# Kernel tuning notes

Hardware: AMD Instinct MI355X
Metric: run time of the kernel (lower is better)

## Reference

```python
import jax, jax.numpy as jnp
import numpy as np

G = 56          # voxel grid resolution per axis
N = 65536
K = 27          # 3x3x3 kernel offsets
C_IN = 128
C_OUT = 128


def _build_rulebook():
    """Submanifold conv rulebook: for each kernel offset, (input_row, output_row) pairs.

    Padded to P=N pairs per offset; invalid pairs use in_idx=0 and out_idx=N
    (a dummy output slot that is dropped), so shapes are static.
    """
    rng = np.random.default_rng(0)
    keys = np.sort(rng.choice(G ** 3, size=N, replace=False)).astype(np.int64)
    x = keys // (G * G)
    y = (keys // G) % G
    z = keys % G
    in_idx = np.zeros((K, N), dtype=np.int32)
    out_idx = np.full((K, N), N, dtype=np.int32)
    k = 0
    for dx in (-1, 0, 1):
        for dy in (-1, 0, 1):
            for dz in (-1, 0, 1):
                nx, ny, nz = x + dx, y + dy, z + dz
                valid = (nx >= 0) & (nx < G) & (ny >= 0) & (ny < G) & (nz >= 0) & (nz < G)
                nkey = (nx * G + ny) * G + nz
                pos = np.searchsorted(keys, np.clip(nkey, 0, G ** 3 - 1))
                pos = np.clip(pos, 0, N - 1)
                found = valid & (keys[pos] == nkey)
                cnt = int(found.sum())
                in_idx[k, :cnt] = pos[found]
                out_idx[k, :cnt] = np.nonzero(found)[0]
                k += 1
    return jnp.asarray(in_idx), jnp.asarray(out_idx)


def setup_inputs() -> dict:
    key = jax.random.key(0)
    k1, k2, k3 = jax.random.split(key, 3)
    fan_in = K * C_IN
    features = jax.random.normal(k1, (N, C_IN), dtype=jnp.float32)
    weight = jax.random.normal(k2, (K, C_IN, C_OUT), dtype=jnp.float32) * (1.0 / np.sqrt(fan_in))
    bias = jax.random.normal(k3, (C_OUT,), dtype=jnp.float32) * 0.01
    in_idx, out_idx = _build_rulebook()
    return {"features": features, "weight": weight, "bias": bias,
            "in_idx": in_idx, "out_idx": out_idx}


def reference(features, weight, bias, in_idx, out_idx):
    # gather: [K, P, C_in]
    gathered = features[in_idx]
    # per-offset GEMM: [K, P, C_out]
    contrib = jnp.einsum('kpc,kcd->kpd', gathered, weight)
    n = features.shape[0]
    c_out = weight.shape[-1]
    # scatter-accumulate into N real rows + 1 dummy row for padded pairs
    out = jnp.zeros((n + 1, c_out), dtype=features.dtype)
    out = out.at[out_idx.reshape(-1)].add(contrib.reshape(-1, c_out))
    return out[:n] + bias
```

## Files before the change

### kernel.cpp

```cpp
#include <hip/hip_runtime.h>
#include <hip/hip_bf16.h>
#include <stdint.h>

#define NV   65536
#define KOFF 27
#define CIN  128
#define COUT 128

typedef __bf16 bf16x8 __attribute__((ext_vector_type(8)));
typedef float  f32x4  __attribute__((ext_vector_type(4)));

__device__ __forceinline__ void async_copy16(void* lds, const void* g) {
    __builtin_amdgcn_global_load_lds(
        (const __attribute__((address_space(1))) void*)g,
        (__attribute__((address_space(3))) void*)lds,
        16, 0, 0);
}

#define JOB_A_BLOCKS 4097
#define JOB_B_BLOCKS 432
#define JOB_S_BLOCKS 1728

__global__ void k_prep_all(const float* __restrict__ f,
                           uint4* __restrict__ fb4,
                           const float* __restrict__ w,
                           uint4* __restrict__ wfrag4,
                           const int4* __restrict__ in4,
                           const int4* __restrict__ out4,
                           int* __restrict__ nbr) {
    const int b = blockIdx.x;
    const int t = threadIdx.x;
    if (b < JOB_A_BLOCKS) {
        int i = b * 256 + t;
        int total8  = (NV + 1) * CIN / 8;
        int nvalid8 = NV * CIN / 8;
        if (i >= total8) return;
        union { uint4 u; __hip_bfloat16 h[8]; } p;
        if (i < nvalid8) {
            const float4* f4 = (const float4*)f;
            float4 a = f4[i * 2];
            float4 c = f4[i * 2 + 1];
            p.h[0] = __float2bfloat16(a.x);
            p.h[1] = __float2bfloat16(a.y);
            p.h[2] = __float2bfloat16(a.z);
            p.h[3] = __float2bfloat16(a.w);
            p.h[4] = __float2bfloat16(c.x);
            p.h[5] = __float2bfloat16(c.y);
            p.h[6] = __float2bfloat16(c.z);
            p.h[7] = __float2bfloat16(c.w);
        } else {
            p.u = make_uint4(0, 0, 0, 0);
        }
        fb4[i] = p.u;
    } else if (b < JOB_A_BLOCKS + JOB_B_BLOCKS) {
        int c    = (b - JOB_A_BLOCKS) * 256 + t;
        int lane = c & 63;
        int nt   = (c >> 6) & 3;
        int wv   = (c >> 8) & 3;
        int s    = c >> 10;
        int ks   = s & 3;
        int k    = s >> 2;
        int cout = (wv & 1) * 64 + nt * 16 + (lane & 15);
        int cin0 = ks * 32 + (lane >> 4) * 8;
        const float* wk = w + k * 16384;
        union { uint4 u; __hip_bfloat16 h[8]; } p;
        #pragma unroll
        for (int j = 0; j < 8; ++j)
            p.h[j] = __float2bfloat16(wk[(cin0 + j) * 128 + cout]);
        wfrag4[c] = p.u;
    } else {
        int i = (b - JOB_A_BLOCKS - JOB_B_BLOCKS) * 256 + t;
        int k = i >> 14;
        int4 ii = in4[i];
        int4 oo = out4[i];
        int* nb = nbr + k * (NV + 1);
        nb[oo.x] = ii.x;
        nb[oo.y] = ii.y;
        nb[oo.z] = ii.z;
        nb[oo.w] = ii.w;
    }
}

__global__ __launch_bounds__(256, 2)
void sp_conv_main(const __hip_bfloat16* __restrict__ feats,
                  const uint4* __restrict__ wfrag,
                  const int* __restrict__ nbr,
                  const float* __restrict__ bias,
                  float* __restrict__ out) {
    __shared__ unsigned char smem[65536];

    const int t   = threadIdx.x;
    const int bid = blockIdx.x;
    const int tile0 = ((bid & 7) * 64 + (bid >> 3)) * 128;

    const int w    = t >> 6;
    const int lane = t & 63;
    const int lr   = lane & 15;
    const int quad = lane >> 4;
    const int m0   = (w >> 1) * 64;
    const int n0   = (w & 1) * 64;

    const int srow   = t >> 4;
    const int sbyte  = ((t & 15) ^ srow) * 16;

    f32x4 acc[4][4] = {};

    const unsigned char* featsB = (const unsigned char*)feats;

    int arows[8];
    {
        const int* nbr0 = nbr + tile0;
        #pragma unroll
        for (int i = 0; i < 8; ++i) arows[i] = nbr0[i * 16 + srow];
    }
    #pragma unroll
    for (int i = 0; i < 8; ++i) {
        unsigned ar = min((unsigned)arows[i], (unsigned)NV);
        async_copy16(smem + i * 4096 + t * 16,
                     featsB + (size_t)ar * 256 + sbyte);
    }
    {
        const int* nbr1 = nbr + (NV + 1) + tile0;
        #pragma unroll
        for (int i = 0; i < 8; ++i) arows[i] = nbr1[i * 16 + srow];
    }
    const uint4* wfp = wfrag + w * 256 + lane;
    uint4 bb[2][4];
    #pragma unroll
    for (int nt = 0; nt < 4; ++nt) bb[0][nt] = wfp[nt * 64];
    __syncthreads();

    int cbuf = 0;
    for (int k = 0; k < KOFF; ++k) {
        if (k + 1 < KOFF) {
            unsigned char* dst = smem + (cbuf ^ 1) * 32768;
            #pragma unroll
            for (int i = 0; i < 8; ++i) {
                unsigned ar = min((unsigned)arows[i], (unsigned)NV);
                async_copy16(dst + i * 4096 + t * 16,
                             featsB + (size_t)ar * 256 + sbyte);
            }
            if (k + 2 < KOFF) {
                const int* nbrn = nbr + (k + 2) * (NV + 1) + tile0;
                #pragma unroll
                for (int i = 0; i < 8; ++i) arows[i] = nbrn[i * 16 + srow];
            }
        }

        const unsigned char* base = smem + cbuf * 32768;
        #pragma unroll
        for (int ks = 0; ks < 4; ++ks) {
            const int s = k * 4 + ks;
            if (s + 1 < 4 * KOFF) {
                const uint4* wfn = wfp + (size_t)(s + 1) * 1024;
                #pragma unroll
                for (int nt = 0; nt < 4; ++nt)
                    bb[(ks + 1) & 1][nt] = wfn[nt * 64];
            }
            bf16x8 af[4];
            #pragma unroll
            for (int mt = 0; mt < 4; ++mt) {
                int row = m0 + mt * 16 + lr;
                af[mt] = *(const bf16x8*)(base + row * 256 +
                                          (((ks * 4 + quad) ^ lr) * 16));
            }
            #pragma unroll
            for (int mt = 0; mt < 4; ++mt)
                #pragma unroll
                for (int nt = 0; nt < 4; ++nt)
                    acc[mt][nt] = __builtin_amdgcn_mfma_f32_16x16x32_bf16(
                        af[mt], *(const bf16x8*)&bb[ks & 1][nt],
                        acc[mt][nt], 0, 0, 0);
        }
        __syncthreads();
        cbuf ^= 1;
    }

    float bv[4];
    #pragma unroll
    for (int nt = 0; nt < 4; ++nt) bv[nt] = bias[n0 + nt * 16 + lr];

    #pragma unroll
    for (int mt = 0; mt < 4; ++mt) {
        #pragma unroll
        for (int nt = 0; nt < 4; ++nt) {
            #pragma unroll
            for (int r = 0; r < 4; ++r) {
                int grow = tile0 + m0 + mt * 16 + quad * 4 + r;
                out[(size_t)grow * COUT + n0 + nt * 16 + lr] =
                    acc[mt][nt][r] + bv[nt];
            }
        }
    }
}


extern "C" void kernel_launch(void* const* d_in, const int* in_sizes, int n_in,
                              void* d_out, int out_size, void* d_ws, size_t ws_size,
                              hipStream_t stream) {
    const float* features = (const float*)d_in[0];
    const float* weight   = (const float*)d_in[1];
    const float* bias     = (const float*)d_in[2];
    const int*   in_idx   = (const int*)d_in[3];
    const int*   out_idx  = (const int*)d_in[4];
    float* out = (float*)d_out;

    uint8_t* ws = (uint8_t*)d_ws;
    size_t off = 0;
    __hip_bfloat16* feats_bf = (__hip_bfloat16*)(ws + off);
    off += (size_t)(NV + 1) * CIN * 2;
    off = (off + 255) & ~(size_t)255;
    uint4* wfrag = (uint4*)(ws + off);
    off += (size_t)(4 * KOFF) * 1024 * 16;
    off = (off + 255) & ~(size_t)255;
    int* nbr = (int*)(ws + off);

    hipMemsetAsync(nbr, 0xFF, (size_t)KOFF * (NV + 1) * 4, stream);

    k_prep_all<<<JOB_A_BLOCKS + JOB_B_BLOCKS + JOB_S_BLOCKS, 256, 0, stream>>>(
        features, (uint4*)feats_bf, weight, wfrag,
        (const int4*)in_idx, (const int4*)out_idx, nbr);

    sp_conv_main<<<NV / 128, 256, 0, stream>>>(feats_bf, wfrag, nbr, bias, out);
}
```

Measured before the change: 165.7 us.

## Prefetch whole-offset weight fragments a stage ahead and dedupe weight layout

The weight fragment buffer drops its duplicated copies for the two waves sharing an N-half, which halves the prep work and workspace. The main loop is unrolled by two with ping-pong register buffers. All four k-slices of the next offset's weight fragments are loaded one offset ahead instead of one k-slice ahead, hiding more global-load latency behind the MFMAs. In exchange, register use roughly quadruples for B fragments (32 uint4 per thread), which risks spills or lower occupancy under launch_bounds(256,2).

```diff
diff --git a/kernel.cpp b/kernel.cpp
--- a/kernel.cpp
+++ b/kernel.cpp
@@ -18,7 +18,7 @@
 }
 
 #define JOB_A_BLOCKS 4097
-#define JOB_B_BLOCKS 432
+#define JOB_B_BLOCKS 216
 #define JOB_S_BLOCKS 1728
 
 __global__ void k_prep_all(const float* __restrict__ f,
@@ -56,11 +56,11 @@
         int c    = (b - JOB_A_BLOCKS) * 256 + t;
         int lane = c & 63;
         int nt   = (c >> 6) & 3;
-        int wv   = (c >> 8) & 3;
-        int s    = c >> 10;
+        int wh   = (c >> 8) & 1;
+        int s    = c >> 9;
         int ks   = s & 3;
         int k    = s >> 2;
-        int cout = (wv & 1) * 64 + nt * 16 + (lane & 15);
+        int cout = wh * 64 + nt * 16 + (lane & 15);
         int cin0 = ks * 32 + (lane >> 4) * 8;
         const float* wk = w + k * 16384;
         union { uint4 u; __hip_bfloat16 h[8]; } p;
@@ -106,8 +106,11 @@
     f32x4 acc[4][4] = {};
 
     const unsigned char* featsB = (const unsigned char*)feats;
-
+    const uint4* wfp = wfrag + (w & 1) * 256 + lane;
+
+    uint4 bb0[4][4], bb1[4][4];
     int arows[8];
+
     {
         const int* nbr0 = nbr + tile0;
         #pragma unroll
@@ -124,57 +127,59 @@
         #pragma unroll
         for (int i = 0; i < 8; ++i) arows[i] = nbr1[i * 16 + srow];
     }
-    const uint4* wfp = wfrag + w * 256 + lane;
-    uint4 bb[2][4];
-    #pragma unroll
-    for (int nt = 0; nt < 4; ++nt) bb[0][nt] = wfp[nt * 64];
+    #pragma unroll
+    for (int ks = 0; ks < 4; ++ks)
+        #pragma unroll
+        for (int nt = 0; nt < 4; ++nt)
+            bb0[ks][nt] = wfp[(size_t)ks * 512 + nt * 64];
     __syncthreads();
 
-    int cbuf = 0;
-    for (int k = 0; k < KOFF; ++k) {
-        if (k + 1 < KOFF) {
-            unsigned char* dst = smem + (cbuf ^ 1) * 32768;
-            #pragma unroll
-            for (int i = 0; i < 8; ++i) {
-                unsigned ar = min((unsigned)arows[i], (unsigned)NV);
-                async_copy16(dst + i * 4096 + t * 16,
-                             featsB + (size_t)ar * 256 + sbyte);
-            }
-            if (k + 2 < KOFF) {
-                const int* nbrn = nbr + (k + 2) * (NV + 1) + tile0;
-                #pragma unroll
-                for (int i = 0; i < 8; ++i) arows[i] = nbrn[i * 16 + srow];
-            }
-        }
-
-        const unsigned char* base = smem + cbuf * 32768;
-        #pragma unroll
-        for (int ks = 0; ks < 4; ++ks) {
-            const int s = k * 4 + ks;
-            if (s + 1 < 4 * KOFF) {
-                const uint4* wfn = wfp + (size_t)(s + 1) * 1024;
-                #pragma unroll
-                for (int nt = 0; nt < 4; ++nt)
-                    bb[(ks + 1) & 1][nt] = wfn[nt * 64];
-            }
-            bf16x8 af[4];
-            #pragma unroll
-            for (int mt = 0; mt < 4; ++mt) {
-                int row = m0 + mt * 16 + lr;
-                af[mt] = *(const bf16x8*)(base + row * 256 +
-                                          (((ks * 4 + quad) ^ lr) * 16));
-            }
-            #pragma unroll
-            for (int mt = 0; mt < 4; ++mt)
-                #pragma unroll
-                for (int nt = 0; nt < 4; ++nt)
-                    acc[mt][nt] = __builtin_amdgcn_mfma_f32_16x16x32_bf16(
-                        af[mt], *(const bf16x8*)&bb[ks & 1][nt],
-                        acc[mt][nt], 0, 0, 0);
-        }
-        __syncthreads();
-        cbuf ^= 1;
-    }
+#define BODY(K, PBUF, CUR, NXT)                                               \
+    do {                                                                      \
+        if ((K) + 1 < KOFF) {                                                 \
+            unsigned char* dst = smem + ((PBUF) ^ 1) * 32768;                 \
+            _Pragma("unroll")                                                 \
+            for (int i = 0; i < 8; ++i) {                                     \
+                unsigned ar = min((unsigned)arows[i], (unsigned)NV);          \
+                async_copy16(dst + i * 4096 + t * 16,                         \
+                             featsB + (size_t)ar * 256 + sbyte);              \
+            }                                                                 \
+            if ((K) + 2 < KOFF) {                                             \
+                const int* nbrn = nbr + ((K) + 2) * (NV + 1) + tile0;         \
+                _Pragma("unroll")                                             \
+                for (int i = 0; i < 8; ++i) arows[i] = nbrn[i * 16 + srow];   \
+            }                                                                 \
+            const uint4* wfn = wfp + (size_t)((K) + 1) * 2048;                \
+            _Pragma("unroll")                                                 \
+            for (int ks = 0; ks < 4; ++ks)                                    \
+                _Pragma("unroll")                                             \
+                for (int nt = 0; nt < 4; ++nt)                                \
+                    NXT[ks][nt] = wfn[(size_t)ks * 512 + nt * 64];            \
+        }                                                                     \
+        const unsigned char* base = smem + (PBUF) * 32768;                    \
+        _Pragma("unroll")                                                     \
+        for (int ks = 0; ks < 4; ++ks) {                                      \
+            _Pragma("unroll")                                                 \
+            for (int mt = 0; mt < 4; ++mt) {                                  \
+                int row = m0 + mt * 16 + lr;                                  \
+                bf16x8 af = *(const bf16x8*)(base + row * 256 +               \
+                                             (((ks * 4 + quad) ^ lr) * 16));  \
+                _Pragma("unroll")                                             \
+                for (int nt = 0; nt < 4; ++nt)                                \
+                    acc[mt][nt] = __builtin_amdgcn_mfma_f32_16x16x32_bf16(    \
+                        af, *(const bf16x8*)&CUR[ks][nt],                     \
+                        acc[mt][nt], 0, 0, 0);                                \
+            }                                                                 \
+        }                                                                     \
+        __syncthreads();                                                      \
+    } while (0)
+
+    for (int kk = 0; kk < KOFF - 1; kk += 2) {
+        BODY(kk,     0, bb0, bb1);
+        BODY(kk + 1, 1, bb1, bb0);
+    }
+    BODY(KOFF - 1, 0, bb0, bb1);
+#undef BODY
 
     float bv[4];
     #pragma unroll
@@ -211,7 +216,7 @@
     off += (size_t)(NV + 1) * CIN * 2;
     off = (off + 255) & ~(size_t)255;
     uint4* wfrag = (uint4*)(ws + off);
-    off += (size_t)(4 * KOFF) * 1024 * 16;
+    off += (size_t)108 * 512 * 16;
     off = (off + 255) & ~(size_t)255;
     int* nbr = (int*)(ws + off);
 
```

New measurement: 162.4 us. 1.02x faster.
